# Kernel tuning notes

Measured on AMD Instinct MI355X. Metric: run time of the kernel, lower is better.

## Reference

```python
import jax, jax.numpy as jnp
import numpy as np

N = 50000      # nodes
E = 800000     # edges (avg degree 16)
F_IN = 32
H = 64         # hidden_features
E_DIM = 16     # edge_dim
C_OUT = 40
L = 2          # num_layers
G = 64         # graphs in batch
BN_EPS = 1e-5
GEN_EPS = 1e-7  # PyG GENConv message eps


def setup_inputs() -> dict:
    key = jax.random.key(0)
    ks = jax.random.split(key, 12)
    s = 0.05
    inp = {}
    inp["x"] = jax.random.normal(ks[0], (N, F_IN), jnp.float32)
    inp["edge_index"] = jax.random.randint(ks[1], (2, E), 0, N)
    inp["edge_attr"] = jax.random.normal(ks[2], (E, E_DIM), jnp.float32)
    inp["batch"] = jnp.sort(jax.random.randint(ks[3], (N,), 0, G))
    # input linear
    inp["lin_in_w"] = jax.random.normal(ks[4], (F_IN, H), jnp.float32) * s
    inp["lin_in_b"] = jnp.zeros((H,), jnp.float32)
    # per-layer DeepGCNLayer norm (BatchNorm affine)
    inp["norm_gamma"] = jnp.ones((L, H), jnp.float32)
    inp["norm_beta"] = jnp.zeros((L, H), jnp.float32)
    # per-layer GENConv params
    inp["edge_w"] = jax.random.normal(ks[5], (L, E_DIM, H), jnp.float32) * s
    inp["edge_b"] = jnp.zeros((L, H), jnp.float32)
    inp["t"] = jnp.ones((L,), jnp.float32)  # learned softmax temperature
    inp["mlp_w1"] = jax.random.normal(ks[6], (L, H, 2 * H), jnp.float32) * s
    inp["mlp_b1"] = jnp.zeros((L, 2 * H), jnp.float32)
    inp["mlp_gamma"] = jnp.ones((L, 2 * H), jnp.float32)
    inp["mlp_beta"] = jnp.zeros((L, 2 * H), jnp.float32)
    inp["mlp_w2"] = jax.random.normal(ks[7], (L, 2 * H, H), jnp.float32) * s
    inp["mlp_b2"] = jnp.zeros((L, H), jnp.float32)
    # output linear
    inp["lin_out_w"] = jax.random.normal(ks[8], (H, C_OUT), jnp.float32) * s
    inp["lin_out_b"] = jnp.zeros((C_OUT,), jnp.float32)
    return inp


def _batch_norm(x, gamma, beta):
    mu = jnp.mean(x, axis=0)
    var = jnp.var(x, axis=0)
    return (x - mu) * jax.lax.rsqrt(var + BN_EPS) * gamma + beta


def _gen_conv(x, src, dst, e_emb, t, w1, b1, g1, be1, w2, b2):
    # message: relu(x_j + edge_emb) + eps   -> [E, H]
    m = jax.nn.relu(x[src] + e_emb) + GEN_EPS
    # softmax aggregation over destination neighborhoods with temperature t
    logits = m * t
    seg_max = jax.ops.segment_max(logits, dst, num_segments=N)      # [N, H]
    ex = jnp.exp(logits - seg_max[dst])                              # [E, H]
    denom = jax.ops.segment_sum(ex, dst, num_segments=N)            # [N, H]
    agg = jax.ops.segment_sum(ex * m, dst, num_segments=N) / (denom + 1e-16)
    # root add, then GENConv MLP: Linear(H,2H) -> BN -> ReLU -> Linear(2H,H)
    out = agg + x
    h = out @ w1 + b1
    h = jax.nn.relu(_batch_norm(h, g1, be1))
    return h @ w2 + b2


def reference(x, edge_index, edge_attr, batch, lin_in_w, lin_in_b,
              norm_gamma, norm_beta, edge_w, edge_b, t,
              mlp_w1, mlp_b1, mlp_gamma, mlp_beta, mlp_w2, mlp_b2,
              lin_out_w, lin_out_b):
    src, dst = edge_index[0], edge_index[1]
    h = x @ lin_in_w + lin_in_b                                      # [N, H]
    for l in range(L):
        # DeepGCNLayer res+ : norm -> act -> (dropout p=0) -> conv, residual add
        z = jax.nn.relu(_batch_norm(h, norm_gamma[l], norm_beta[l]))
        e_emb = edge_attr @ edge_w[l] + edge_b[l]                    # [E, H]
        c = _gen_conv(z, src, dst, e_emb, t[l], mlp_w1[l], mlp_b1[l],
                      mlp_gamma[l], mlp_beta[l], mlp_w2[l], mlp_b2[l])
        h = h + c
    # global mean pool per graph
    sums = jax.ops.segment_sum(h, batch, num_segments=G)             # [G, H]
    counts = jax.ops.segment_sum(jnp.ones((N, 1), h.dtype), batch, num_segments=G)
    pooled = sums / jnp.maximum(counts, 1.0)
    out = jax.nn.relu(pooled) @ lin_out_w + lin_out_b                # [G, C_OUT]
    return out
```

## Files before the change

kernel.cpp:

```cpp
#include <hip/hip_runtime.h>

#define N_NODES 50000
#define N_EDGES 800000
#define F_INP   32
#define HDIM    64
#define EDIM    16
#define COUT    40
#define NGRAPH  64

__global__ void hist_kernel(const int* __restrict__ dst, int* __restrict__ cnt, int E) {
    int e = blockIdx.x * 256 + threadIdx.x;
    if (e < E) atomicAdd(&cnt[dst[e]], 1);
}

__global__ void scan_part_kernel(const int* __restrict__ cnt, int* __restrict__ bsum, int n) {
    __shared__ int red[256];
    int tid = threadIdx.x;
    int idx = blockIdx.x * 256 + tid;
    red[tid] = (idx < n) ? cnt[idx] : 0;
    __syncthreads();
    for (int off = 128; off > 0; off >>= 1) {
        if (tid < off) red[tid] += red[tid + off];
        __syncthreads();
    }
    if (tid == 0) bsum[blockIdx.x] = red[0];
}

__global__ void scan_top_kernel(int* __restrict__ bsum, int nb) {
    __shared__ int tmp[256];
    int tid = threadIdx.x;
    int v = (tid < nb) ? bsum[tid] : 0;
    tmp[tid] = v;
    __syncthreads();
    for (int off = 1; off < 256; off <<= 1) {
        int x = (tid >= off) ? tmp[tid - off] : 0;
        __syncthreads();
        tmp[tid] += x;
        __syncthreads();
    }
    if (tid < nb) bsum[tid] = tmp[tid] - v;
}

__global__ void scan_apply_kernel(const int* __restrict__ cnt, const int* __restrict__ bsum,
                                  int* __restrict__ offsets, int* __restrict__ cursor, int n) {
    __shared__ int tmp[256];
    int tid = threadIdx.x;
    int idx = blockIdx.x * 256 + tid;
    int v = (idx < n) ? cnt[idx] : 0;
    tmp[tid] = v;
    __syncthreads();
    for (int off = 1; off < 256; off <<= 1) {
        int x = (tid >= off) ? tmp[tid - off] : 0;
        __syncthreads();
        tmp[tid] += x;
        __syncthreads();
    }
    int excl = tmp[tid] - v + bsum[blockIdx.x];
    if (idx < n) { offsets[idx] = excl; cursor[idx] = excl; }
    if (idx == n - 1) offsets[n] = excl + v;
}

__global__ void scatter_kernel(const int* __restrict__ dst, int* __restrict__ cursor,
                               int* __restrict__ sorted, int E) {
    int e = blockIdx.x * 256 + threadIdx.x;
    if (e < E) {
        int p = atomicAdd(&cursor[dst[e]], 1);
        sorted[p] = e;
    }
}

__global__ void gstart_kernel(const int* __restrict__ batch, int* __restrict__ gstart,
                              int N, int G) {
    int n = blockIdx.x * 256 + threadIdx.x;
    if (n >= N) return;
    int g  = batch[n];
    int gp = (n == 0) ? -1 : batch[n - 1];
    for (int gg = gp + 1; gg <= g; gg++) gstart[gg] = n;
    if (n == N - 1) {
        for (int gg = g + 1; gg <= G; gg++) gstart[gg] = N;
    }
}

__global__ void lin_in_kernel(const float* __restrict__ x, const float* __restrict__ W,
                              const float* __restrict__ b, float* __restrict__ h, int N) {
    int tid = threadIdx.x;
    int c = tid & 63;
    float w[F_INP];
#pragma unroll
    for (int k = 0; k < F_INP; k++) w[k] = W[k * HDIM + c];
    int node = blockIdx.x * 4 + (tid >> 6);
    if (node >= N) return;
    const float4* xr = (const float4*)(x + (size_t)node * F_INP);
    float acc = b[c];
#pragma unroll
    for (int k4 = 0; k4 < F_INP / 4; k4++) {
        float4 xv = xr[k4];
        acc += xv.x * w[k4 * 4 + 0] + xv.y * w[k4 * 4 + 1]
             + xv.z * w[k4 * 4 + 2] + xv.w * w[k4 * 4 + 3];
    }
    h[(size_t)node * HDIM + c] = acc;
}

template <int C>
__global__ void bn_stats_kernel(const float* __restrict__ x, float* __restrict__ stats, int N) {
    const int RPB = 256 / C;
    int tid = threadIdx.x;
    int c = tid % C;
    int row0 = blockIdx.x * RPB + tid / C;
    int stride = gridDim.x * RPB;
    float s = 0.f, ss = 0.f;
    for (int r = row0; r < N; r += stride) {
        float v = x[(size_t)r * C + c];
        s += v; ss += v * v;
    }
    __shared__ float ls[256], lss[256];
    ls[tid] = s; lss[tid] = ss;
    __syncthreads();
    if (tid < C) {
        for (int k = 1; k < RPB; k++) { s += ls[tid + k * C]; ss += lss[tid + k * C]; }
        atomicAdd(&stats[c], s);
        atomicAdd(&stats[C + c], ss);
    }
}

__global__ void agg_kernel(const float* __restrict__ h, const int* __restrict__ src,
                           const float* __restrict__ ea, const float* __restrict__ We,
                           const float* __restrict__ be, const float* __restrict__ tptr,
                           const float* __restrict__ stats,
                           const float* __restrict__ gamma, const float* __restrict__ beta,
                           const int* __restrict__ offsets, const int* __restrict__ sorted,
                           float* __restrict__ out, int N) {
    int tid = threadIdx.x;
    int c = tid & 63;
    float inv = 1.0f / (float)N;
    float mu  = stats[c] * inv;
    float var = stats[HDIM + c] * inv - mu * mu;
    float rs  = rsqrtf(var + 1e-5f);
    float ga  = gamma[c], bb = beta[c];
    float w[EDIM];
#pragma unroll
    for (int k = 0; k < EDIM; k++) w[k] = We[k * HDIM + c];
    float bc = be[c];
    float tval = *tptr;

    int wid = __builtin_amdgcn_readfirstlane(tid >> 6);
    int node = blockIdx.x * 4 + wid;
    if (node >= N) return;
    int beg = offsets[node], end = offsets[node + 1];
    int deg = end - beg;

    float denom = 0.f, num = 0.f;
    if (deg > 0) {
        int e0 = sorted[beg];
        int s0 = src[e0];
        int e1, s1;
        if (deg > 1) { e1 = sorted[beg + 1]; s1 = src[e1]; }
        else         { e1 = e0;              s1 = s0; }

        float a[EDIM];
        {
            const float* ar = ea + (size_t)e0 * EDIM;
#pragma unroll
            for (int k = 0; k < EDIM; k++) a[k] = ar[k];
        }
        float hv = h[(size_t)s0 * HDIM + c];

        for (int j = 0; j < deg - 1; j++) {
            float an[EDIM];
            {
                const float* arn = ea + (size_t)e1 * EDIM;
#pragma unroll
                for (int k = 0; k < EDIM; k++) an[k] = arn[k];
            }
            float hn = h[(size_t)s1 * HDIM + c];
            int nxt = (j + 2 < deg) ? (j + 2) : (deg - 1);
            int e2 = sorted[beg + nxt];
            int s2 = src[e2];

            float acc = bc;
#pragma unroll
            for (int k = 0; k < EDIM; k++) acc += a[k] * w[k];
            float zv = fmaxf((hv - mu) * rs * ga + bb, 0.f);
            float m  = fmaxf(zv + acc, 0.f) + 1e-7f;
            float ex = __expf(m * tval);
            denom += ex;
            num   += ex * m;

#pragma unroll
            for (int k = 0; k < EDIM; k++) a[k] = an[k];
            hv = hn; e1 = e2; s1 = s2;
        }
        {
            float acc = bc;
#pragma unroll
            for (int k = 0; k < EDIM; k++) acc += a[k] * w[k];
            float zv = fmaxf((hv - mu) * rs * ga + bb, 0.f);
            float m  = fmaxf(zv + acc, 0.f) + 1e-7f;
            float ex = __expf(m * tval);
            denom += ex;
            num   += ex * m;
        }
    }
    float hvn = h[(size_t)node * HDIM + c];
    float zn = fmaxf((hvn - mu) * rs * ga + bb, 0.f);
    out[(size_t)node * HDIM + c] = num / (denom + 1e-16f) + zn;
}

__global__ __launch_bounds__(256) void mlp1_kernel(
        const float* __restrict__ in, const float* __restrict__ W1,
        const float* __restrict__ b1, float* __restrict__ h1, int N) {
    __shared__ float sW[HDIM * 128];
    __shared__ float srow[32 * 65];
    int tid = threadIdx.x;
    for (int i = tid; i < HDIM * 128; i += 256) sW[i] = W1[i];
    int base = blockIdx.x * 32;
    for (int i = tid; i < 32 * HDIM; i += 256) {
        int r = i >> 6, cc = i & 63;
        int node = base + r;
        srow[r * 65 + cc] = (node < N) ? in[(size_t)node * HDIM + cc] : 0.f;
    }
    __syncthreads();
    int tx = tid & 31;
    int ty = tid >> 5;
    float acc[4][4];
    float b0 = b1[4 * tx], bb1 = b1[4 * tx + 1], b2v = b1[4 * tx + 2], b3 = b1[4 * tx + 3];
#pragma unroll
    for (int j = 0; j < 4; j++) { acc[j][0] = b0; acc[j][1] = bb1; acc[j][2] = b2v; acc[j][3] = b3; }
#pragma unroll 8
    for (int k = 0; k < HDIM; k++) {
        float4 wv = *(const float4*)&sW[k * 128 + 4 * tx];
        float r0 = srow[(ty * 4 + 0) * 65 + k];
        float r1 = srow[(ty * 4 + 1) * 65 + k];
        float r2 = srow[(ty * 4 + 2) * 65 + k];
        float r3 = srow[(ty * 4 + 3) * 65 + k];
        acc[0][0] += r0 * wv.x; acc[0][1] += r0 * wv.y; acc[0][2] += r0 * wv.z; acc[0][3] += r0 * wv.w;
        acc[1][0] += r1 * wv.x; acc[1][1] += r1 * wv.y; acc[1][2] += r1 * wv.z; acc[1][3] += r1 * wv.w;
        acc[2][0] += r2 * wv.x; acc[2][1] += r2 * wv.y; acc[2][2] += r2 * wv.z; acc[2][3] += r2 * wv.w;
        acc[3][0] += r3 * wv.x; acc[3][1] += r3 * wv.y; acc[3][2] += r3 * wv.z; acc[3][3] += r3 * wv.w;
    }
#pragma unroll
    for (int j = 0; j < 4; j++) {
        int node = base + ty * 4 + j;
        if (node < N)
            *(float4*)&h1[(size_t)node * 128 + 4 * tx] =
                make_float4(acc[j][0], acc[j][1], acc[j][2], acc[j][3]);
    }
}

__global__ __launch_bounds__(256) void mlp2_kernel(
        const float* __restrict__ h1, const float* __restrict__ stats,
        const float* __restrict__ mg, const float* __restrict__ mb,
        const float* __restrict__ W2, const float* __restrict__ b2,
        float* __restrict__ h, int N) {
    __shared__ float sW[128 * HDIM];
    __shared__ float sact[32 * 129];
    __shared__ float sbn[4 * 128];
    int tid = threadIdx.x;
    for (int i = tid; i < 128 * HDIM; i += 256) sW[i] = W2[i];
    if (tid < 128) {
        float inv = 1.0f / (float)N;
        float mu  = stats[tid] * inv;
        float var = stats[128 + tid] * inv - mu * mu;
        sbn[tid]       = mu;
        sbn[128 + tid] = rsqrtf(var + 1e-5f);
        sbn[256 + tid] = mg[tid];
        sbn[384 + tid] = mb[tid];
    }
    __syncthreads();
    int base = blockIdx.x * 32;
    for (int i = tid; i < 32 * 128; i += 256) {
        int r = i >> 7, o = i & 127;
        int node = base + r;
        float v = 0.f;
        if (node < N) {
            v = h1[(size_t)node * 128 + o];
            v = fmaxf((v - sbn[o]) * sbn[128 + o] * sbn[256 + o] + sbn[384 + o], 0.f);
        }
        sact[r * 129 + o] = v;
    }
    __syncthreads();
    int tx = tid & 15;
    int ty = tid >> 4;
    float acc[2][4];
    float b0 = b2[4 * tx], bb1 = b2[4 * tx + 1], b2v = b2[4 * tx + 2], b3 = b2[4 * tx + 3];
    acc[0][0] = b0; acc[0][1] = bb1; acc[0][2] = b2v; acc[0][3] = b3;
    acc[1][0] = b0; acc[1][1] = bb1; acc[1][2] = b2v; acc[1][3] = b3;
#pragma unroll 8
    for (int k = 0; k < 128; k++) {
        float4 wv = *(const float4*)&sW[k * HDIM + 4 * tx];
        float r0 = sact[(ty * 2 + 0) * 129 + k];
        float r1 = sact[(ty * 2 + 1) * 129 + k];
        acc[0][0] += r0 * wv.x; acc[0][1] += r0 * wv.y; acc[0][2] += r0 * wv.z; acc[0][3] += r0 * wv.w;
        acc[1][0] += r1 * wv.x; acc[1][1] += r1 * wv.y; acc[1][2] += r1 * wv.z; acc[1][3] += r1 * wv.w;
    }
#pragma unroll
    for (int j = 0; j < 2; j++) {
        int node = base + ty * 2 + j;
        if (node < N) {
            float4* p = (float4*)&h[(size_t)node * HDIM + 4 * tx];
            float4 old = *p;
            *p = make_float4(old.x + acc[j][0], old.y + acc[j][1],
                             old.z + acc[j][2], old.w + acc[j][3]);
        }
    }
}

__global__ void pool_out_kernel(const float* __restrict__ h, const int* __restrict__ gstart,
                                const float* __restrict__ Wo, const float* __restrict__ bo,
                                float* __restrict__ out, int N) {
    __shared__ float sp[HDIM];
    __shared__ float red[256];
    __shared__ float sW[HDIM * COUT];
    int g = blockIdx.x;
    int tid = threadIdx.x;
    for (int i = tid; i < HDIM * COUT; i += 256) sW[i] = Wo[i];
    int beg = gstart[g], end = gstart[g + 1];
    int c = tid & 63, r0 = tid >> 6;
    float s = 0.f;
    for (int r = beg + r0; r < end; r += 4) s += h[(size_t)r * HDIM + c];
    red[tid] = s;
    __syncthreads();
    if (tid < HDIM) {
        s = red[tid] + red[tid + 64] + red[tid + 128] + red[tid + 192];
        float cnt = (float)(end - beg);
        float pooled = s / fmaxf(cnt, 1.0f);
        sp[tid] = fmaxf(pooled, 0.0f);
    }
    __syncthreads();
    if (tid < COUT) {
        float acc = bo[tid];
#pragma unroll
        for (int k = 0; k < HDIM; k++) acc += sp[k] * sW[k * COUT + tid];
        out[g * COUT + tid] = acc;
    }
}

extern "C" void kernel_launch(void* const* d_in, const int* in_sizes, int n_in,
                              void* d_out, int out_size, void* d_ws, size_t ws_size,
                              hipStream_t stream) {
    (void)in_sizes; (void)n_in; (void)out_size; (void)ws_size;
    const float* x          = (const float*)d_in[0];
    const int*   eidx       = (const int*)  d_in[1];
    const float* eattr      = (const float*)d_in[2];
    const int*   batch      = (const int*)  d_in[3];
    const float* lin_in_w   = (const float*)d_in[4];
    const float* lin_in_b   = (const float*)d_in[5];
    const float* norm_gamma = (const float*)d_in[6];
    const float* norm_beta  = (const float*)d_in[7];
    const float* edge_w     = (const float*)d_in[8];
    const float* edge_b     = (const float*)d_in[9];
    const float* tparam     = (const float*)d_in[10];
    const float* mlp_w1     = (const float*)d_in[11];
    const float* mlp_b1     = (const float*)d_in[12];
    const float* mlp_gamma  = (const float*)d_in[13];
    const float* mlp_beta   = (const float*)d_in[14];
    const float* mlp_w2     = (const float*)d_in[15];
    const float* mlp_b2     = (const float*)d_in[16];
    const float* lin_out_w  = (const float*)d_in[17];
    const float* lin_out_b  = (const float*)d_in[18];
    float* out = (float*)d_out;

    const int* src = eidx;
    const int* dst = eidx + N_EDGES;

    char* ws = (char*)d_ws;
    size_t off = 0;
    auto alloc = [&](size_t bytes) -> char* {
        char* p = ws + off;
        off = (off + bytes + 255) & ~(size_t)255;
        return p;
    };
    int*   cnt     = (int*)  alloc((size_t)N_NODES * 4);
    float* statsA0 = (float*)alloc(128 * 4);
    float* statsB0 = (float*)alloc(256 * 4);
    float* statsA1 = (float*)alloc(128 * 4);
    float* statsB1 = (float*)alloc(256 * 4);
    size_t zero_bytes = off;
    int*   bsum    = (int*)  alloc(256 * 4);
    int*   offsets = (int*)  alloc((size_t)(N_NODES + 1) * 4);
    int*   cursor  = (int*)  alloc((size_t)N_NODES * 4);
    int*   sorted  = (int*)  alloc((size_t)N_EDGES * 4);
    int*   gstart  = (int*)  alloc((size_t)(NGRAPH + 1) * 4);
    float* h       = (float*)alloc((size_t)N_NODES * HDIM * 4);
    float* ob      = (float*)alloc((size_t)N_NODES * HDIM * 4);
    float* h1      = (float*)alloc((size_t)N_NODES * 2 * HDIM * 4);

    hipMemsetAsync(d_ws, 0, zero_bytes, stream);

    const int NB = (N_NODES + 255) / 256;
    hist_kernel      <<<(N_EDGES + 255) / 256, 256, 0, stream>>>(dst, cnt, N_EDGES);
    scan_part_kernel <<<NB, 256, 0, stream>>>(cnt, bsum, N_NODES);
    scan_top_kernel  <<<1, 256, 0, stream>>>(bsum, NB);
    scan_apply_kernel<<<NB, 256, 0, stream>>>(cnt, bsum, offsets, cursor, N_NODES);
    scatter_kernel   <<<(N_EDGES + 255) / 256, 256, 0, stream>>>(dst, cursor, sorted, N_EDGES);
    gstart_kernel    <<<NB, 256, 0, stream>>>(batch, gstart, N_NODES, NGRAPH);
    lin_in_kernel    <<<(N_NODES + 3) / 4, 256, 0, stream>>>(x, lin_in_w, lin_in_b, h, N_NODES);

    float* statsA[2] = { statsA0, statsA1 };
    float* statsB[2] = { statsB0, statsB1 };
    for (int l = 0; l < 2; l++) {
        bn_stats_kernel<64><<<256, 256, 0, stream>>>(h, statsA[l], N_NODES);
        agg_kernel<<<(N_NODES + 3) / 4, 256, 0, stream>>>(
            h, src, eattr, edge_w + (size_t)l * EDIM * HDIM, edge_b + l * HDIM,
            tparam + l, statsA[l], norm_gamma + l * HDIM, norm_beta + l * HDIM,
            offsets, sorted, ob, N_NODES);
        mlp1_kernel<<<(N_NODES + 31) / 32, 256, 0, stream>>>(
            ob, mlp_w1 + (size_t)l * HDIM * 2 * HDIM, mlp_b1 + l * 2 * HDIM, h1, N_NODES);
        bn_stats_kernel<128><<<256, 256, 0, stream>>>(h1, statsB[l], N_NODES);
        mlp2_kernel<<<(N_NODES + 31) / 32, 256, 0, stream>>>(
            h1, statsB[l], mlp_gamma + l * 2 * HDIM, mlp_beta + l * 2 * HDIM,
            mlp_w2 + (size_t)l * 2 * HDIM * HDIM, mlp_b2 + l * HDIM, h, N_NODES);
    }
    pool_out_kernel<<<NGRAPH, 256, 0, stream>>>(h, gstart, lin_out_w, lin_out_b, out, N_NODES);
}
```

Measured before the change: 703.8 us.

## Switch softmax aggregation to edge-balanced chunks with atomic segment flush

Replaces the one-wave-per-node aggregation with fixed chunks of 128 dst-sorted edges per wave. Each wave accumulates the softmax numerator and denominator per destination run and flushes them with atomics into num/den buffers. The division and the residual with the normalized self feature move into mlp1's load stage. This aims to even out load across skewed degrees and avoid idle waves, at the cost of atomics, an extra memset, an extra dsts array, and doubled intermediate traffic. It relies on N_EDGES being a multiple of CHUNK and on the unstabilized exp without the max subtraction, as before.

```diff
diff --git a/kernel.cpp b/kernel.cpp
--- a/kernel.cpp
+++ b/kernel.cpp
@@ -7,6 +7,7 @@
 #define EDIM    16
 #define COUT    40
 #define NGRAPH  64
+#define CHUNK   128
 
 __global__ void hist_kernel(const int* __restrict__ dst, int* __restrict__ cnt, int E) {
     int e = blockIdx.x * 256 + threadIdx.x;
@@ -61,11 +62,13 @@
 }
 
 __global__ void scatter_kernel(const int* __restrict__ dst, int* __restrict__ cursor,
-                               int* __restrict__ sorted, int E) {
+                               int* __restrict__ sorted, int* __restrict__ dsts, int E) {
     int e = blockIdx.x * 256 + threadIdx.x;
     if (e < E) {
-        int p = atomicAdd(&cursor[dst[e]], 1);
+        int d = dst[e];
+        int p = atomicAdd(&cursor[d], 1);
         sorted[p] = e;
+        dsts[p]   = d;
     }
 }
 
@@ -123,16 +126,17 @@
     }
 }
 
-__global__ void agg_kernel(const float* __restrict__ h, const int* __restrict__ src,
-                           const float* __restrict__ ea, const float* __restrict__ We,
-                           const float* __restrict__ be, const float* __restrict__ tptr,
-                           const float* __restrict__ stats,
-                           const float* __restrict__ gamma, const float* __restrict__ beta,
-                           const int* __restrict__ offsets, const int* __restrict__ sorted,
-                           float* __restrict__ out, int N) {
+__global__ __launch_bounds__(256) void edge_agg_kernel(
+        const float* __restrict__ h, const int* __restrict__ src,
+        const float* __restrict__ ea, const float* __restrict__ We,
+        const float* __restrict__ be, const float* __restrict__ tptr,
+        const float* __restrict__ stats,
+        const float* __restrict__ gamma, const float* __restrict__ beta,
+        const int* __restrict__ sorted, const int* __restrict__ dsts,
+        float* __restrict__ num, float* __restrict__ den, int E) {
     int tid = threadIdx.x;
     int c = tid & 63;
-    float inv = 1.0f / (float)N;
+    float inv = 1.0f / (float)N_NODES;
     float mu  = stats[c] * inv;
     float var = stats[HDIM + c] * inv - mu * mu;
     float rs  = rsqrtf(var + 1e-5f);
@@ -143,81 +147,105 @@
     float bc = be[c];
     float tval = *tptr;
 
-    int wid = __builtin_amdgcn_readfirstlane(tid >> 6);
-    int node = blockIdx.x * 4 + wid;
-    if (node >= N) return;
-    int beg = offsets[node], end = offsets[node + 1];
-    int deg = end - beg;
-
-    float denom = 0.f, num = 0.f;
-    if (deg > 0) {
-        int e0 = sorted[beg];
-        int s0 = src[e0];
-        int e1, s1;
-        if (deg > 1) { e1 = sorted[beg + 1]; s1 = src[e1]; }
-        else         { e1 = e0;              s1 = s0; }
-
-        float a[EDIM];
+    int wid = __builtin_amdgcn_readfirstlane((int)(blockIdx.x * 4 + (tid >> 6)));
+    int p0 = wid * CHUNK;
+    if (p0 >= E) return;
+
+    int e0 = sorted[p0];
+    int d0 = dsts[p0];
+    int s0 = src[e0];
+    float a[EDIM];
+    {
+        const float* ar = ea + (size_t)e0 * EDIM;
+#pragma unroll
+        for (int k = 0; k < EDIM; k++) a[k] = ar[k];
+    }
+    float hv = h[(size_t)s0 * HDIM + c];
+
+    int cur_d = d0;
+    float nacc = 0.f, dacc = 0.f;
+
+#pragma unroll 4
+    for (int j = 0; j < CHUNK - 1; j++) {
+        int pn = p0 + j + 1;
+        int e1 = sorted[pn];
+        int d1 = dsts[pn];
+        int s1 = src[e1];
+        float an[EDIM];
         {
-            const float* ar = ea + (size_t)e0 * EDIM;
-#pragma unroll
-            for (int k = 0; k < EDIM; k++) a[k] = ar[k];
+            const float* arn = ea + (size_t)e1 * EDIM;
+#pragma unroll
+            for (int k = 0; k < EDIM; k++) an[k] = arn[k];
         }
-        float hv = h[(size_t)s0 * HDIM + c];
-
-        for (int j = 0; j < deg - 1; j++) {
-            float an[EDIM];
-            {
-                const float* arn = ea + (size_t)e1 * EDIM;
-#pragma unroll
-                for (int k = 0; k < EDIM; k++) an[k] = arn[k];
-            }
-            float hn = h[(size_t)s1 * HDIM + c];
-            int nxt = (j + 2 < deg) ? (j + 2) : (deg - 1);
-            int e2 = sorted[beg + nxt];
-            int s2 = src[e2];
-
-            float acc = bc;
-#pragma unroll
-            for (int k = 0; k < EDIM; k++) acc += a[k] * w[k];
-            float zv = fmaxf((hv - mu) * rs * ga + bb, 0.f);
-            float m  = fmaxf(zv + acc, 0.f) + 1e-7f;
-            float ex = __expf(m * tval);
-            denom += ex;
-            num   += ex * m;
-
-#pragma unroll
-            for (int k = 0; k < EDIM; k++) a[k] = an[k];
-            hv = hn; e1 = e2; s1 = s2;
+        float hn = h[(size_t)s1 * HDIM + c];
+
+        if (d0 != cur_d) {
+            atomicAdd(&num[(size_t)cur_d * HDIM + c], nacc);
+            atomicAdd(&den[(size_t)cur_d * HDIM + c], dacc);
+            cur_d = d0; nacc = 0.f; dacc = 0.f;
         }
-        {
-            float acc = bc;
-#pragma unroll
-            for (int k = 0; k < EDIM; k++) acc += a[k] * w[k];
-            float zv = fmaxf((hv - mu) * rs * ga + bb, 0.f);
-            float m  = fmaxf(zv + acc, 0.f) + 1e-7f;
-            float ex = __expf(m * tval);
-            denom += ex;
-            num   += ex * m;
-        }
-    }
-    float hvn = h[(size_t)node * HDIM + c];
-    float zn = fmaxf((hvn - mu) * rs * ga + bb, 0.f);
-    out[(size_t)node * HDIM + c] = num / (denom + 1e-16f) + zn;
+        float acc = bc;
+#pragma unroll
+        for (int k = 0; k < EDIM; k++) acc += a[k] * w[k];
+        float zv = fmaxf((hv - mu) * rs * ga + bb, 0.f);
+        float m  = fmaxf(zv + acc, 0.f) + 1e-7f;
+        float ex = __expf(m * tval);
+        dacc += ex;
+        nacc += ex * m;
+
+#pragma unroll
+        for (int k = 0; k < EDIM; k++) a[k] = an[k];
+        hv = hn; d0 = d1; s0 = s1;
+    }
+    if (d0 != cur_d) {
+        atomicAdd(&num[(size_t)cur_d * HDIM + c], nacc);
+        atomicAdd(&den[(size_t)cur_d * HDIM + c], dacc);
+        cur_d = d0; nacc = 0.f; dacc = 0.f;
+    }
+    {
+        float acc = bc;
+#pragma unroll
+        for (int k = 0; k < EDIM; k++) acc += a[k] * w[k];
+        float zv = fmaxf((hv - mu) * rs * ga + bb, 0.f);
+        float m  = fmaxf(zv + acc, 0.f) + 1e-7f;
+        float ex = __expf(m * tval);
+        dacc += ex;
+        nacc += ex * m;
+    }
+    atomicAdd(&num[(size_t)cur_d * HDIM + c], nacc);
+    atomicAdd(&den[(size_t)cur_d * HDIM + c], dacc);
 }
 
 __global__ __launch_bounds__(256) void mlp1_kernel(
-        const float* __restrict__ in, const float* __restrict__ W1,
-        const float* __restrict__ b1, float* __restrict__ h1, int N) {
+        const float* __restrict__ num, const float* __restrict__ den,
+        const float* __restrict__ h, const float* __restrict__ stats,
+        const float* __restrict__ gamma, const float* __restrict__ beta,
+        const float* __restrict__ W1, const float* __restrict__ b1,
+        float* __restrict__ h1, int N) {
     __shared__ float sW[HDIM * 128];
     __shared__ float srow[32 * 65];
     int tid = threadIdx.x;
     for (int i = tid; i < HDIM * 128; i += 256) sW[i] = W1[i];
     int base = blockIdx.x * 32;
-    for (int i = tid; i < 32 * HDIM; i += 256) {
-        int r = i >> 6, cc = i & 63;
-        int node = base + r;
-        srow[r * 65 + cc] = (node < N) ? in[(size_t)node * HDIM + cc] : 0.f;
+    {
+        int cc = tid & 63;
+        float inv = 1.0f / (float)N_NODES;
+        float mu  = stats[cc] * inv;
+        float var = stats[HDIM + cc] * inv - mu * mu;
+        float rs  = rsqrtf(var + 1e-5f);
+        float ga  = gamma[cc], bb = beta[cc];
+        for (int i = tid; i < 32 * HDIM; i += 256) {
+            int r = i >> 6;
+            int node = base + r;
+            float v = 0.f;
+            if (node < N) {
+                size_t idx = (size_t)node * HDIM + cc;
+                float hv = h[idx];
+                float z  = fmaxf((hv - mu) * rs * ga + bb, 0.f);
+                v = num[idx] / (den[idx] + 1e-16f) + z;
+            }
+            srow[r * 65 + cc] = v;
+        }
     }
     __syncthreads();
     int tx = tid & 31;
@@ -380,9 +408,11 @@
     int*   offsets = (int*)  alloc((size_t)(N_NODES + 1) * 4);
     int*   cursor  = (int*)  alloc((size_t)N_NODES * 4);
     int*   sorted  = (int*)  alloc((size_t)N_EDGES * 4);
+    int*   dsts    = (int*)  alloc((size_t)N_EDGES * 4);
     int*   gstart  = (int*)  alloc((size_t)(NGRAPH + 1) * 4);
     float* h       = (float*)alloc((size_t)N_NODES * HDIM * 4);
-    float* ob      = (float*)alloc((size_t)N_NODES * HDIM * 4);
+    float* num     = (float*)alloc((size_t)N_NODES * HDIM * 4);
+    float* den     = (float*)alloc((size_t)N_NODES * HDIM * 4);
     float* h1      = (float*)alloc((size_t)N_NODES * 2 * HDIM * 4);
 
     hipMemsetAsync(d_ws, 0, zero_bytes, stream);
@@ -392,20 +422,25 @@
     scan_part_kernel <<<NB, 256, 0, stream>>>(cnt, bsum, N_NODES);
     scan_top_kernel  <<<1, 256, 0, stream>>>(bsum, NB);
     scan_apply_kernel<<<NB, 256, 0, stream>>>(cnt, bsum, offsets, cursor, N_NODES);
-    scatter_kernel   <<<(N_EDGES + 255) / 256, 256, 0, stream>>>(dst, cursor, sorted, N_EDGES);
+    scatter_kernel   <<<(N_EDGES + 255) / 256, 256, 0, stream>>>(dst, cursor, sorted, dsts, N_EDGES);
     gstart_kernel    <<<NB, 256, 0, stream>>>(batch, gstart, N_NODES, NGRAPH);
     lin_in_kernel    <<<(N_NODES + 3) / 4, 256, 0, stream>>>(x, lin_in_w, lin_in_b, h, N_NODES);
+
+    const int NWAVE = N_EDGES / CHUNK;
+    const int AGG_BLOCKS = (NWAVE + 3) / 4;
 
     float* statsA[2] = { statsA0, statsA1 };
     float* statsB[2] = { statsB0, statsB1 };
     for (int l = 0; l < 2; l++) {
+        hipMemsetAsync(num, 0, (size_t)N_NODES * HDIM * 4 * 2, stream);
         bn_stats_kernel<64><<<256, 256, 0, stream>>>(h, statsA[l], N_NODES);
-        agg_kernel<<<(N_NODES + 3) / 4, 256, 0, stream>>>(
+        edge_agg_kernel<<<AGG_BLOCKS, 256, 0, stream>>>(
             h, src, eattr, edge_w + (size_t)l * EDIM * HDIM, edge_b + l * HDIM,
             tparam + l, statsA[l], norm_gamma + l * HDIM, norm_beta + l * HDIM,
-            offsets, sorted, ob, N_NODES);
+            sorted, dsts, num, den, N_EDGES);
         mlp1_kernel<<<(N_NODES + 31) / 32, 256, 0, stream>>>(
-            ob, mlp_w1 + (size_t)l * HDIM * 2 * HDIM, mlp_b1 + l * 2 * HDIM, h1, N_NODES);
+            num, den, h, statsA[l], norm_gamma + l * HDIM, norm_beta + l * HDIM,
+            mlp_w1 + (size_t)l * HDIM * 2 * HDIM, mlp_b1 + l * 2 * HDIM, h1, N_NODES);
         bn_stats_kernel<128><<<256, 256, 0, stream>>>(h1, statsB[l], N_NODES);
         mlp2_kernel<<<(N_NODES + 31) / 32, 256, 0, stream>>>(
             h1, statsB[l], mlp_gamma + l * 2 * HDIM, mlp_beta + l * 2 * HDIM,
```

Measured after the change: 838.0 us. 19.1% more time.
